# Kernel tuning notes

Measured on AMD Instinct MI355X. Metric: run time of the kernel, lower is better.

The kernel has to match this reference:

```python
import jax, jax.numpy as jnp
import numpy as np

EPS = 1e-07  # DIoULoss eps


def setup_inputs() -> dict:
    key = jax.random.key(0)
    k1, k2, k3, k4, k5 = jax.random.split(key, 5)
    B, Q = 32, 131072
    # valid xyxy boxes: uniform centers in [0,100), sizes in [1,51)
    def make_boxes(kc, ks):
        c = jax.random.uniform(kc, (B, Q, 2), dtype=jnp.float32) * 100.0
        wh = jax.random.uniform(ks, (B, Q, 2), dtype=jnp.float32) * 50.0 + 1.0
        return jnp.concatenate([c - wh / 2, c + wh / 2], axis=-1)
    inputs = make_boxes(k1, k2)
    targets = make_boxes(k3, k4)
    mask = jax.random.randint(k5, (B, Q), 0, 2).astype(jnp.bool_)
    num_boxes = 2097152
    return {"inputs": inputs, "targets": targets, "mask": mask, "num_boxes": num_boxes}


def _diou_loss(b1, b2):
    # b1, b2: (N, 4) xyxy. Per-pair GIoU == diagonal of the original NxN matrix.
    a1 = (b1[:, 2] - b1[:, 0]) * (b1[:, 3] - b1[:, 1])
    a2 = (b2[:, 2] - b2[:, 0]) * (b2[:, 3] - b2[:, 1])
    lt = jnp.maximum(b1[:, :2], b2[:, :2])
    rb = jnp.minimum(b1[:, 2:], b2[:, 2:])
    wh = jnp.clip(rb - lt, 0.0)
    inter = wh[:, 0] * wh[:, 1]
    union = a1 + a2 - inter
    iou = inter / union
    lt_c = jnp.minimum(b1[:, :2], b2[:, :2])
    rb_c = jnp.maximum(b1[:, 2:], b2[:, 2:])
    wh_c = rb_c - lt_c  # boxes are valid so enclose extent >= 0
    area_c = wh_c[:, 0] * wh_c[:, 1]
    giou = iou - (area_c - union) / area_c
    # DIoU penalty: squared center distance / squared enclosing diagonal
    c1 = (b1[:, :2] + b1[:, 2:]) * 0.5
    c2 = (b2[:, :2] + b2[:, 2:]) * 0.5
    d2 = jnp.sum((c1 - c2) ** 2, axis=1)
    diag2 = wh_c[:, 0] ** 2 + wh_c[:, 1] ** 2
    diou = giou - d2 / (diag2 + EPS)
    return 1.0 - diou


def reference(inputs, targets, mask, num_boxes):
    B, Q, _ = inputs.shape
    loss = _diou_loss(inputs.reshape(-1, 4), targets.reshape(-1, 4)).reshape(B, Q)
    loss = loss * mask.astype(loss.dtype)
    # reduction='mean' with num_boxes provided -> sum / num_boxes
    return loss.sum() / num_boxes
```

## Files before the change

### kernel.cpp

```cpp
#include <hip/hip_runtime.h>

#define DIOU_EPS 1e-7f

constexpr int BLOCK = 256;
constexpr int ITEMS = 8;
constexpr int CHUNK = BLOCK * ITEMS;

__global__ void zero_out_kernel(float* out) {
    out[0] = 0.0f;
}

__device__ __forceinline__ float rcp_fast(float x) {
    return __builtin_amdgcn_rcpf(x);
}

__device__ __forceinline__ float diou_elem(float4 a, float4 b, int m) {
    float a1 = (a.z - a.x) * (a.w - a.y);
    float a2 = (b.z - b.x) * (b.w - b.y);

    float iw = fmaxf(fminf(a.z, b.z) - fmaxf(a.x, b.x), 0.0f);
    float ih = fmaxf(fminf(a.w, b.w) - fmaxf(a.y, b.y), 0.0f);
    float inter = iw * ih;
    float uni = a1 + a2 - inter;

    float wc = fmaxf(a.z, b.z) - fminf(a.x, b.x);
    float hc = fmaxf(a.w, b.w) - fminf(a.y, b.y);
    float area_c = wc * hc;

    float dx = (a.x + a.z - b.x - b.z) * 0.5f;
    float dy = (a.y + a.w - b.y - b.w) * 0.5f;
    float d2 = dx * dx + dy * dy;
    float diag2 = wc * wc + hc * hc;

    float iou_term  = inter * rcp_fast(uni);
    float giou_term = uni * rcp_fast(area_c);
    float pen_term  = d2 * rcp_fast(diag2 + DIOU_EPS);
    float loss = 2.0f - iou_term - giou_term + pen_term;

    float mf = (m != 0) ? 1.0f : 0.0f;
    return mf * loss;
}

__global__ __launch_bounds__(BLOCK) void diou_loss_kernel(
    const float4* __restrict__ boxes1,
    const float4* __restrict__ boxes2,
    const int* __restrict__ mask,
    const int* __restrict__ num_boxes,
    float* __restrict__ out,
    int n)
{
    const int t = threadIdx.x;
    const int base = blockIdx.x * CHUNK;

    float acc = 0.0f;

    if (base + CHUNK <= n) {
        float4 A[ITEMS], B[ITEMS];
        int    M[ITEMS];
        #pragma unroll
        for (int j = 0; j < ITEMS; ++j) A[j] = boxes1[base + j * BLOCK + t];
        #pragma unroll
        for (int j = 0; j < ITEMS; ++j) B[j] = boxes2[base + j * BLOCK + t];
        #pragma unroll
        for (int j = 0; j < ITEMS; ++j) M[j] = mask[base + j * BLOCK + t];

        __builtin_amdgcn_sched_barrier(0);

        #pragma unroll
        for (int j = 0; j < ITEMS; ++j) acc += diou_elem(A[j], B[j], M[j]);
    } else {
        for (int j = 0; j < ITEMS; ++j) {
            int i = base + j * BLOCK + t;
            if (i < n) acc += diou_elem(boxes1[i], boxes2[i], mask[i]);
        }
    }

    #pragma unroll
    for (int off = 32; off > 0; off >>= 1)
        acc += __shfl_down(acc, off, 64);

    __shared__ float wave_sums[BLOCK / 64];
    int wave = t >> 6;
    if ((t & 63) == 0) wave_sums[wave] = acc;
    __syncthreads();

    if (t == 0) {
        float s = wave_sums[0] + wave_sums[1] + wave_sums[2] + wave_sums[3];
        float inv_nb = 1.0f / (float)num_boxes[0];
        atomicAdd(out, s * inv_nb);
    }
}

extern "C" void kernel_launch(void* const* d_in, const int* in_sizes, int n_in,
                              void* d_out, int out_size, void* d_ws, size_t ws_size,
                              hipStream_t stream) {
    const float4* boxes1 = (const float4*)d_in[0];
    const float4* boxes2 = (const float4*)d_in[1];
    const int* mask = (const int*)d_in[2];
    const int* num_boxes = (const int*)d_in[3];

    float* out = (float*)d_out;
    int n = in_sizes[2];

    zero_out_kernel<<<1, 1, 0, stream>>>(out);

    int grid = (n + CHUNK - 1) / CHUNK;
    diou_loss_kernel<<<grid, BLOCK, 0, stream>>>(boxes1, boxes2, mask, num_boxes, out, n);
}
```

Before: 164.1 us.

## Stage box and mask loads through LDS with direct global-to-LDS DMA

Global loads of both box arrays and the mask are replaced with 16-byte global_load_lds transfers into shared memory, split across waves in 1 KB chunks, followed by a barrier and compute from LDS. Items per thread drop from 8 to 4, which doubles the number of blocks. The intent is to bypass VGPR staging, cut register pressure and raise memory-level parallelism for this bandwidth-bound reduction. The cost is about 36 KB of LDS per block, which may limit occupancy, plus an extra barrier and more atomics.

```diff
diff --git a/kernel.cpp b/kernel.cpp
--- a/kernel.cpp
+++ b/kernel.cpp
@@ -3,8 +3,19 @@
 #define DIOU_EPS 1e-7f
 
 constexpr int BLOCK = 256;
-constexpr int ITEMS = 8;
+constexpr int ITEMS = 4;
 constexpr int CHUNK = BLOCK * ITEMS;
+
+constexpr int A_CHUNKS = CHUNK * 16 / 1024;
+constexpr int B_CHUNKS = CHUNK * 16 / 1024;
+constexpr int M_CHUNKS = CHUNK * 4 / 1024;
+constexpr int N_CHUNKS = A_CHUNKS + B_CHUNKS + M_CHUNKS;
+constexpr int CHUNKS_PER_WAVE = N_CHUNKS / 4;
+
+#define GLOBAL_TO_LDS16(g, l)                                                  \
+    __builtin_amdgcn_global_load_lds(                                          \
+        (const __attribute__((address_space(1))) void*)(g),                    \
+        (__attribute__((address_space(3))) void*)(l), 16, 0, 0)
 
 __global__ void zero_out_kernel(float* out) {
     out[0] = 0.0f;
@@ -32,13 +43,11 @@
     float d2 = dx * dx + dy * dy;
     float diag2 = wc * wc + hc * hc;
 
-    float iou_term  = inter * rcp_fast(uni);
-    float giou_term = uni * rcp_fast(area_c);
-    float pen_term  = d2 * rcp_fast(diag2 + DIOU_EPS);
-    float loss = 2.0f - iou_term - giou_term + pen_term;
+    float loss = 2.0f - inter * rcp_fast(uni)
+                      - uni   * rcp_fast(area_c)
+                      + d2    * rcp_fast(diag2 + DIOU_EPS);
 
-    float mf = (m != 0) ? 1.0f : 0.0f;
-    return mf * loss;
+    return (m != 0) ? loss : 0.0f;
 }
 
 __global__ __launch_bounds__(BLOCK) void diou_loss_kernel(
@@ -49,39 +58,65 @@
     float* __restrict__ out,
     int n)
 {
-    const int t = threadIdx.x;
-    const int base = blockIdx.x * CHUNK;
+    __shared__ float4 Alds[CHUNK];
+    __shared__ float4 Blds[CHUNK];
+    __shared__ int    Mlds[CHUNK];
+    __shared__ float  wave_sums[BLOCK / 64];
+
+    const int t    = threadIdx.x;
+    const int lane = t & 63;
+    const int wave = t >> 6;
+    const long long base = (long long)blockIdx.x * CHUNK;
 
     float acc = 0.0f;
 
     if (base + CHUNK <= n) {
-        float4 A[ITEMS], B[ITEMS];
-        int    M[ITEMS];
-        #pragma unroll
-        for (int j = 0; j < ITEMS; ++j) A[j] = boxes1[base + j * BLOCK + t];
-        #pragma unroll
-        for (int j = 0; j < ITEMS; ++j) B[j] = boxes2[base + j * BLOCK + t];
-        #pragma unroll
-        for (int j = 0; j < ITEMS; ++j) M[j] = mask[base + j * BLOCK + t];
-
-        __builtin_amdgcn_sched_barrier(0);
+        const char* Ag = (const char*)(boxes1 + base);
+        const char* Bg = (const char*)(boxes2 + base);
+        const char* Mg = (const char*)(mask + base);
+        char* Al = (char*)&Alds[0];
+        char* Bl = (char*)&Blds[0];
+        char* Ml = (char*)&Mlds[0];
 
         #pragma unroll
-        for (int j = 0; j < ITEMS; ++j) acc += diou_elem(A[j], B[j], M[j]);
+        for (int k = 0; k < CHUNKS_PER_WAVE; ++k) {
+            int c = wave * CHUNKS_PER_WAVE + k;
+            const char* g;
+            char* l;
+            if (c < A_CHUNKS) {
+                g = Ag + c * 1024;
+                l = Al + c * 1024;
+            } else if (c < A_CHUNKS + B_CHUNKS) {
+                int cc = c - A_CHUNKS;
+                g = Bg + cc * 1024;
+                l = Bl + cc * 1024;
+            } else {
+                int cc = c - A_CHUNKS - B_CHUNKS;
+                g = Mg + cc * 1024;
+                l = Ml + cc * 1024;
+            }
+            GLOBAL_TO_LDS16(g + lane * 16, l);
+        }
+        __syncthreads();
+
+        #pragma unroll
+        for (int j = 0; j < ITEMS; ++j) {
+            int e = j * BLOCK + t;
+            acc += diou_elem(Alds[e], Blds[e], Mlds[e]);
+        }
     } else {
         for (int j = 0; j < ITEMS; ++j) {
-            int i = base + j * BLOCK + t;
+            long long i = base + j * BLOCK + t;
             if (i < n) acc += diou_elem(boxes1[i], boxes2[i], mask[i]);
         }
+        __syncthreads();
     }
 
     #pragma unroll
     for (int off = 32; off > 0; off >>= 1)
         acc += __shfl_down(acc, off, 64);
 
-    __shared__ float wave_sums[BLOCK / 64];
-    int wave = t >> 6;
-    if ((t & 63) == 0) wave_sums[wave] = acc;
+    if (lane == 0) wave_sums[wave] = acc;
     __syncthreads();
 
     if (t == 0) {
```

Result: slower. 178.4 us (+8.7%).
